# Optimization experiments

Hardware: AMD Instinct MI355X
Metric: run time of the kernel (lower is better)

Reference implementation:

```python
import jax, jax.numpy as jnp
import numpy as np

B, T, N, C = 2, 12, 4096, 32
FILTERS = [32, 32, 32]


def setup_inputs() -> dict:
    key = jax.random.key(0)
    ks = jax.random.split(key, 12)
    inp = {
        'data': jax.random.normal(ks[0], (B, T, N, C), dtype=jnp.float32),
        'adj': jax.random.uniform(ks[1], (3 * N, 3 * N), dtype=jnp.float32) / (3.0 * N),
        'temporal_emb': jax.random.normal(ks[2], (1, T, 1, C), dtype=jnp.float32) * 0.0003,
        'spatial_emb': jax.random.normal(ks[3], (1, 1, N, C), dtype=jnp.float32) * 0.0003,
    }
    c_in = C
    for i, f in enumerate(FILTERS):
        scale = 1.0 / np.sqrt(c_in)
        inp[f'W{i}'] = jax.random.uniform(ks[4 + 2 * i], (c_in, 2 * f), dtype=jnp.float32,
                                          minval=-scale, maxval=scale)
        inp[f'b{i}'] = jnp.zeros((2 * f,), dtype=jnp.float32)
        c_in = f
    return inp


def reference(data, adj, temporal_emb, spatial_emb, W0, b0, W1, b1, W2, b2):
    # data: (B, T, N, C). Add temporal + spatial position embeddings.
    x = data + temporal_emb + spatial_emb
    b, t, n, c = x.shape
    w = t - 2  # number of sliding windows
    # Gather all 3-step windows at once: (B, W, 3, N, C) -> (B, W, 3N, C)
    idx = jnp.arange(w)[:, None] + jnp.arange(3)[None, :]
    xw = x[:, idx].reshape(b, w, 3 * n, c)
    outs = []
    for Wl, bl in ((W0, b0), (W1, b1), (W2, b2)):
        # dense graph conv over the 3N local graph, batched over (B, W)
        xw = jnp.einsum('nm,bwmc->bwnc', adj, xw)
        y = xw @ Wl + bl            # (B, W, 3N, 2*C')
        lhs, rhs = jnp.split(y, 2, axis=-1)
        xw = lhs * jax.nn.sigmoid(rhs)  # GLU, (B, W, 3N, C')
        outs.append(xw[:, :, n:2 * n, :])  # crop middle timestep
    # stacked max over the gcn layers: (B, T-2, N, C_last)
    return jnp.max(jnp.stack(outs, axis=0), axis=0)
```

## Files before the change

kernel.cpp:

```cpp
#include <hip/hip_runtime.h>

#define NN 4096
#define TT 12
#define BB 2
#define CC 32
#define WW 10
#define K3 12288
#define NCOL 640
#define SA 4096.0f
#define SX 1024.0f

typedef _Float16 half8 __attribute__((ext_vector_type(8)));
typedef _Float16 half4_t __attribute__((ext_vector_type(4)));
typedef float floatx4 __attribute__((ext_vector_type(4)));

__global__ void k_conv_adj(const float* __restrict__ adj, _Float16* __restrict__ a16) {
    long n4 = (long)K3 * K3 / 4;
    long i = (long)blockIdx.x * blockDim.x + threadIdx.x;
    long stride = (long)gridDim.x * blockDim.x;
    const float4* src = (const float4*)adj;
    half4_t* dst = (half4_t*)a16;
    for (; i < n4; i += stride) {
        float4 v = src[i];
        half4_t h;
        h[0] = (_Float16)(v.x * SA);
        h[1] = (_Float16)(v.y * SA);
        h[2] = (_Float16)(v.z * SA);
        h[3] = (_Float16)(v.w * SA);
        dst[i] = h;
    }
}

__global__ void k_prep(const float* __restrict__ data, const float* __restrict__ temb,
                       const float* __restrict__ semb, _Float16* __restrict__ x0t) {
    __shared__ float sb[CC][64 + 1];
    int z = blockIdx.y;
    int b = z / 30; int r = z % 30; int w = r / 3; int j = r % 3;
    int t = w + j;
    int n0 = blockIdx.x * 64;
    int tid = threadIdx.x;
    for (int e = tid; e < 64 * CC; e += 256) {
        int nl = e >> 5, c = e & 31;
        float v = data[((long)(b * TT + t) * NN + n0 + nl) * CC + c]
                + temb[t * CC + c] + semb[(n0 + nl) * CC + c];
        sb[c][nl] = v;
    }
    __syncthreads();
    int bw = b * WW + w;
    for (int e = tid; e < 64 * CC; e += 256) {
        int c = e >> 6, nl = e & 63;
        x0t[(long)(bw * CC + c) * K3 + j * NN + n0 + nl] = (_Float16)sb[c][nl];
    }
}

__device__ __forceinline__ void gload_lds16(const _Float16* g, _Float16* l) {
    __builtin_amdgcn_global_load_lds(
        (const __attribute__((address_space(1))) void*)g,
        (__attribute__((address_space(3))) void*)l, 16, 0, 0);
}

__global__ __launch_bounds__(256, 2) void k_gemm(
    const _Float16* __restrict__ A, const _Float16* __restrict__ BT,
    float* __restrict__ G, int K)
{
    __shared__ __attribute__((aligned(16))) _Float16 As[128 * 32];
    __shared__ __attribute__((aligned(16))) _Float16 Bs[128 * 32];

    const int nbn = NCOL / 128;
    int nwg = gridDim.x;
    int cpx = nwg >> 3;
    int bid = blockIdx.x;
    int wg = (bid & 7) * cpx + (bid >> 3);
    int mt = wg / nbn, nt = wg - mt * nbn;
    long m0 = (long)mt * 128; long n0 = nt * 128;

    int tid = threadIdx.x;
    int lane = tid & 63, wid = tid >> 6;
    int wm = wid >> 1, wn = wid & 1;

    int rowS0 = tid >> 2, kb0 = tid & 3;
    int ks0 = kb0 ^ ((rowS0 >> 1) & 3);
    int s1 = tid + 256;
    int rowS1 = s1 >> 2, kb1 = s1 & 3;
    int ks1 = kb1 ^ ((rowS1 >> 1) & 3);

    const _Float16* aSrc0 = A + (m0 + rowS0) * (long)K + ks0 * 8;
    const _Float16* aSrc1 = A + (m0 + rowS1) * (long)K + ks1 * 8;
    const _Float16* bSrc0 = BT + (n0 + rowS0) * (long)K + ks0 * 8;
    const _Float16* bSrc1 = BT + (n0 + rowS1) * (long)K + ks1 * 8;

    floatx4 acc[4][4] = {};

    int arow = wm * 64 + (lane & 15);
    int brow = wn * 64 + (lane & 15);
    int ksr = lane >> 4;
    int kbA = ksr ^ ((arow >> 1) & 3);
    int kbB = ksr ^ ((brow >> 1) & 3);

#pragma unroll 1
    for (int k0 = 0; k0 < K; k0 += 32) {
        __syncthreads();
        gload_lds16(aSrc0 + k0, As + wid * 512);
        gload_lds16(aSrc1 + k0, As + 2048 + wid * 512);
        gload_lds16(bSrc0 + k0, Bs + wid * 512);
        gload_lds16(bSrc1 + k0, Bs + 2048 + wid * 512);
        asm volatile("s_waitcnt vmcnt(0)" ::: "memory");
        __syncthreads();

        half8 af[4], bf[4];
#pragma unroll
        for (int ms = 0; ms < 4; ++ms)
            af[ms] = *(const half8*)(As + (arow + ms * 16) * 32 + kbA * 8);
#pragma unroll
        for (int ns = 0; ns < 4; ++ns)
            bf[ns] = *(const half8*)(Bs + (brow + ns * 16) * 32 + kbB * 8);
#pragma unroll
        for (int ms = 0; ms < 4; ++ms)
#pragma unroll
            for (int ns = 0; ns < 4; ++ns)
                acc[ms][ns] = __builtin_amdgcn_mfma_f32_16x16x32_f16(af[ms], bf[ns], acc[ms][ns], 0, 0, 0);
    }

    int rb = (lane >> 4) * 4;
    int cb = lane & 15;
#pragma unroll
    for (int ms = 0; ms < 4; ++ms) {
        long row = m0 + wm * 64 + ms * 16 + rb;
#pragma unroll
        for (int ns = 0; ns < 4; ++ns) {
            long col = n0 + wn * 64 + ns * 16 + cb;
#pragma unroll
            for (int i = 0; i < 4; ++i)
                G[(row + i) * NCOL + col] = acc[ms][ns][i];
        }
    }
}

template <int MODE>
__global__ __launch_bounds__(256) void k_glu(
    const float* __restrict__ G, const float* __restrict__ Wt,
    const float* __restrict__ bias, _Float16* __restrict__ outH,
    float* __restrict__ outF, float invS, float outScale)
{
    __shared__ float Wl[CC * 64];
    __shared__ float bl[64];
    __shared__ _Float16 tb[4][CC][64];
    int tid = threadIdx.x;
    for (int e = tid; e < CC * 64; e += 256) Wl[e] = Wt[e];
    if (tid < 64) bl[tid] = bias[tid];
    __syncthreads();

    int blk = blockIdx.x;
    int mt = blk / 5, bwt = blk % 5;
    int m0 = mt * 64, bw0 = bwt * 4;
    int ml = tid >> 2, bwl = tid & 3;
    int m = m0 + ml, bw = bw0 + bwl;

    const float* gp = G + (long)m * NCOL + bw * CC;
    float g[CC];
#pragma unroll
    for (int c4 = 0; c4 < CC / 4; ++c4) {
        float4 v = ((const float4*)gp)[c4];
        g[c4 * 4 + 0] = v.x * invS; g[c4 * 4 + 1] = v.y * invS;
        g[c4 * 4 + 2] = v.z * invS; g[c4 * 4 + 3] = v.w * invS;
    }
    float y[64];
#pragma unroll
    for (int o = 0; o < 64; ++o) y[o] = bl[o];
#pragma unroll
    for (int c = 0; c < CC; ++c) {
        float gv = g[c];
#pragma unroll
        for (int o = 0; o < 64; ++o) y[o] = fmaf(gv, Wl[c * 64 + o], y[o]);
    }
    if (MODE == 0) {
#pragma unroll
        for (int c = 0; c < CC; ++c) {
            float r = y[c] * (1.f / (1.f + __expf(-y[c + 32])));
            tb[bwl][c][ml] = (_Float16)(r * outScale);
        }
        __syncthreads();
        for (int e = tid; e < 4 * CC * 64; e += 256) {
            int bwl2 = e >> 11, c2 = (e >> 6) & 31, ml2 = e & 63;
            outH[(long)((bw0 + bwl2) * CC + c2) * K3 + m0 + ml2] = tb[bwl2][c2][ml2];
        }
    } else {
        float* op = outF + (long)m * NCOL + bw * CC;
#pragma unroll
        for (int c = 0; c < CC; ++c) {
            float r = y[c] * (1.f / (1.f + __expf(-y[c + 32])));
            op[c] = r;
        }
    }
}

__global__ void k_final(const _Float16* __restrict__ x1t, const _Float16* __restrict__ x2t,
                        const float* __restrict__ o3, float* __restrict__ out)
{
    __shared__ float sb[64][CC + 1];
    int bw = blockIdx.y;
    int n0 = blockIdx.x * 64;
    int tid = threadIdx.x;
    for (int e = tid; e < CC * 64; e += 256) {
        int c = e >> 6, nl = e & 63;
        long idx = (long)(bw * CC + c) * K3 + NN + n0 + nl;
        float v1 = (float)x1t[idx] * (1.f / SX);
        float v2 = (float)x2t[idx] * (1.f / SX);
        sb[nl][c] = fmaxf(v1, v2);
    }
    __syncthreads();
    for (int e = tid; e < 64 * CC; e += 256) {
        int nl = e >> 5, c = e & 31;
        float v = fmaxf(sb[nl][c], o3[(long)(n0 + nl) * NCOL + bw * CC + c]);
        out[((long)bw * NN + n0 + nl) * CC + c] = v;
    }
}

extern "C" void kernel_launch(void* const* d_in, const int* in_sizes, int n_in,
                              void* d_out, int out_size, void* d_ws, size_t ws_size,
                              hipStream_t stream)
{
    const float* data = (const float*)d_in[0];
    const float* adj  = (const float*)d_in[1];
    const float* temb = (const float*)d_in[2];
    const float* semb = (const float*)d_in[3];
    const float* W0 = (const float*)d_in[4];
    const float* b0 = (const float*)d_in[5];
    const float* W1 = (const float*)d_in[6];
    const float* b1 = (const float*)d_in[7];
    const float* W2 = (const float*)d_in[8];
    const float* b2 = (const float*)d_in[9];
    float* out = (float*)d_out;

    char* ws = (char*)d_ws;
    _Float16* A16 = (_Float16*)ws;  ws += (size_t)K3 * K3 * 2;
    _Float16* X0  = (_Float16*)ws;  ws += (size_t)NCOL * K3 * 2;
    _Float16* X1  = (_Float16*)ws;  ws += (size_t)NCOL * K3 * 2;
    _Float16* X2  = (_Float16*)ws;  ws += (size_t)NCOL * K3 * 2;
    float*    G   = (float*)ws;     ws += (size_t)K3 * NCOL * 4;
    float*    O3  = (float*)ws;     ws += (size_t)NN * NCOL * 4;

    k_conv_adj<<<4096, 256, 0, stream>>>(adj, A16);
    k_prep<<<dim3(64, 60), 256, 0, stream>>>(data, temb, semb, X0);

    k_gemm<<<480, 256, 0, stream>>>(A16, X0, G, K3);
    k_glu<0><<<960, 256, 0, stream>>>(G, W0, b0, X1, nullptr, 1.f / SA, SX);
    k_gemm<<<480, 256, 0, stream>>>(A16, X1, G, K3);
    k_glu<0><<<960, 256, 0, stream>>>(G, W1, b1, X2, nullptr, 1.f / (SA * SX), SX);
    k_gemm<<<160, 256, 0, stream>>>(A16 + (size_t)NN * K3, X2, G, K3);
    k_glu<1><<<320, 256, 0, stream>>>(G, W2, b2, nullptr, O3, 1.f / (SA * SX), 1.f);

    k_final<<<dim3(64, 20), 256, 0, stream>>>(X1, X2, O3, out);
}
```

Measured before the change: 1.090 ms.

## Fuse GEMM with GLU epilogue and final max using full-width N tiles

Replaces the separate GEMM, GLU and final-max kernels with one fused kernel per layer. Each block computes a 48-row by all-640-column tile with double-buffered LDS staging, then runs the GLU weight multiply from LDS scratch and writes fp16 output directly. The last layer also folds in the max over the three layers. This removes the fp32 G round trips and extra launches, and reads A only once per layer instead of once per 128-column tile. In exchange, the grid is only 256 blocks (86 for the last layer) of 512 threads with large LDS use, which may cut occupancy. The LDS swizzle was also dropped, which may cause bank conflicts.

```diff
diff --git a/kernel.cpp b/kernel.cpp
--- a/kernel.cpp
+++ b/kernel.cpp
@@ -9,6 +9,9 @@
 #define NCOL 640
 #define SA 4096.0f
 #define SX 1024.0f
+#define BM 48
+#define BK 32
+#define NT (K3 / BK)
 
 typedef _Float16 half8 __attribute__((ext_vector_type(8)));
 typedef _Float16 half4_t __attribute__((ext_vector_type(4)));
@@ -59,161 +62,135 @@
         (__attribute__((address_space(3))) void*)l, 16, 0, 0);
 }
 
-__global__ __launch_bounds__(256, 2) void k_gemm(
+template <int MODE>
+__global__ __launch_bounds__(512, 2) void k_gemm_glu(
     const _Float16* __restrict__ A, const _Float16* __restrict__ BT,
-    float* __restrict__ G, int K)
+    const float* __restrict__ Wt, const float* __restrict__ bias,
+    _Float16* __restrict__ outH,
+    const _Float16* __restrict__ x1, const _Float16* __restrict__ x2,
+    float* __restrict__ outF,
+    float invS, int Mvalid)
 {
-    __shared__ __attribute__((aligned(16))) _Float16 As[128 * 32];
-    __shared__ __attribute__((aligned(16))) _Float16 Bs[128 * 32];
-
-    const int nbn = NCOL / 128;
-    int nwg = gridDim.x;
-    int cpx = nwg >> 3;
-    int bid = blockIdx.x;
-    int wg = (bid & 7) * cpx + (bid >> 3);
-    int mt = wg / nbn, nt = wg - mt * nbn;
-    long m0 = (long)mt * 128; long n0 = nt * 128;
+    __shared__ __attribute__((aligned(16))) _Float16 AB[2][22016];
+    __shared__ float WB[CC * 64 + 64];
 
     int tid = threadIdx.x;
     int lane = tid & 63, wid = tid >> 6;
-    int wm = wid >> 1, wn = wid & 1;
-
-    int rowS0 = tid >> 2, kb0 = tid & 3;
-    int ks0 = kb0 ^ ((rowS0 >> 1) & 3);
-    int s1 = tid + 256;
-    int rowS1 = s1 >> 2, kb1 = s1 & 3;
-    int ks1 = kb1 ^ ((rowS1 >> 1) & 3);
-
-    const _Float16* aSrc0 = A + (m0 + rowS0) * (long)K + ks0 * 8;
-    const _Float16* aSrc1 = A + (m0 + rowS1) * (long)K + ks1 * 8;
-    const _Float16* bSrc0 = BT + (n0 + rowS0) * (long)K + ks0 * 8;
-    const _Float16* bSrc1 = BT + (n0 + rowS1) * (long)K + ks1 * 8;
-
-    floatx4 acc[4][4] = {};
-
-    int arow = wm * 64 + (lane & 15);
-    int brow = wn * 64 + (lane & 15);
-    int ksr = lane >> 4;
-    int kbA = ksr ^ ((arow >> 1) & 3);
-    int kbB = ksr ^ ((brow >> 1) & 3);
-
+    long m0 = (long)blockIdx.x * BM;
+
+    for (int e = tid; e < CC * 64; e += 512) WB[e] = Wt[e];
+    if (tid < 64) WB[CC * 64 + tid] = bias[tid];
+
+    int rowA = tid >> 2, kbA = tid & 3;
+    const _Float16* aSrc = A + (m0 + rowA) * (long)K3 + kbA * 8;
+    const _Float16* bSrc0 = BT + (long)((0 * 512 + tid) >> 2) * K3 + ((0 * 512 + tid) & 3) * 8;
+    const _Float16* bSrc1 = BT + (long)((1 * 512 + tid) >> 2) * K3 + ((1 * 512 + tid) & 3) * 8;
+    const _Float16* bSrc2 = BT + (long)((2 * 512 + tid) >> 2) * K3 + ((2 * 512 + tid) & 3) * 8;
+    const _Float16* bSrc3 = BT + (long)((3 * 512 + tid) >> 2) * K3 + ((3 * 512 + tid) & 3) * 8;
+    const _Float16* bSrc4 = BT + (long)((4 * 512 + tid) >> 2) * K3 + ((4 * 512 + tid) & 3) * 8;
+
+#define STAGE(bufi, tt)                                                          \
+    do {                                                                         \
+        long k0 = (long)(tt) * BK;                                               \
+        _Float16* bp = AB[bufi];                                                 \
+        gload_lds16(bSrc0 + k0, bp + 1536 + 0 * 4096 + wid * 512);               \
+        gload_lds16(bSrc1 + k0, bp + 1536 + 1 * 4096 + wid * 512);               \
+        gload_lds16(bSrc2 + k0, bp + 1536 + 2 * 4096 + wid * 512);               \
+        gload_lds16(bSrc3 + k0, bp + 1536 + 3 * 4096 + wid * 512);               \
+        gload_lds16(bSrc4 + k0, bp + 1536 + 4 * 4096 + wid * 512);               \
+        if (wid < 3) gload_lds16(aSrc + k0, bp + wid * 512);                     \
+    } while (0)
+
+    floatx4 acc[3][5] = {};
+    int fr = lane & 15;
+    int kq = lane >> 4;
+
+    STAGE(0, 0);
+    asm volatile("s_waitcnt vmcnt(0)" ::: "memory");
+    __syncthreads();
+
+    int cur = 0;
 #pragma unroll 1
-    for (int k0 = 0; k0 < K; k0 += 32) {
-        __syncthreads();
-        gload_lds16(aSrc0 + k0, As + wid * 512);
-        gload_lds16(aSrc1 + k0, As + 2048 + wid * 512);
-        gload_lds16(bSrc0 + k0, Bs + wid * 512);
-        gload_lds16(bSrc1 + k0, Bs + 2048 + wid * 512);
+    for (int t = 0; t < NT; ++t) {
+        if (t != NT - 1) STAGE(cur ^ 1, t + 1);
+        const _Float16* P = AB[cur];
+        half8 af[3], bf[5];
+#pragma unroll
+        for (int ms = 0; ms < 3; ++ms)
+            af[ms] = *(const half8*)(P + (ms * 16 + fr) * 32 + kq * 8);
+#pragma unroll
+        for (int ns = 0; ns < 5; ++ns)
+            bf[ns] = *(const half8*)(P + 1536 + (wid * 80 + ns * 16 + fr) * 32 + kq * 8);
+#pragma unroll
+        for (int ms = 0; ms < 3; ++ms)
+#pragma unroll
+            for (int ns = 0; ns < 5; ++ns)
+                acc[ms][ns] = __builtin_amdgcn_mfma_f32_16x16x32_f16(af[ms], bf[ns], acc[ms][ns], 0, 0, 0);
         asm volatile("s_waitcnt vmcnt(0)" ::: "memory");
         __syncthreads();
-
-        half8 af[4], bf[4];
-#pragma unroll
-        for (int ms = 0; ms < 4; ++ms)
-            af[ms] = *(const half8*)(As + (arow + ms * 16) * 32 + kbA * 8);
-#pragma unroll
-        for (int ns = 0; ns < 4; ++ns)
-            bf[ns] = *(const half8*)(Bs + (brow + ns * 16) * 32 + kbB * 8);
-#pragma unroll
-        for (int ms = 0; ms < 4; ++ms)
-#pragma unroll
-            for (int ns = 0; ns < 4; ++ns)
-                acc[ms][ns] = __builtin_amdgcn_mfma_f32_16x16x32_f16(af[ms], bf[ns], acc[ms][ns], 0, 0, 0);
-    }
-
-    int rb = (lane >> 4) * 4;
-    int cb = lane & 15;
-#pragma unroll
-    for (int ms = 0; ms < 4; ++ms) {
-        long row = m0 + wm * 64 + ms * 16 + rb;
-#pragma unroll
-        for (int ns = 0; ns < 4; ++ns) {
-            long col = n0 + wn * 64 + ns * 16 + cb;
-#pragma unroll
-            for (int i = 0; i < 4; ++i)
-                G[(row + i) * NCOL + col] = acc[ms][ns][i];
-        }
-    }
-}
-
-template <int MODE>
-__global__ __launch_bounds__(256) void k_glu(
-    const float* __restrict__ G, const float* __restrict__ Wt,
-    const float* __restrict__ bias, _Float16* __restrict__ outH,
-    float* __restrict__ outF, float invS, float outScale)
-{
-    __shared__ float Wl[CC * 64];
-    __shared__ float bl[64];
-    __shared__ _Float16 tb[4][CC][64];
-    int tid = threadIdx.x;
-    for (int e = tid; e < CC * 64; e += 256) Wl[e] = Wt[e];
-    if (tid < 64) bl[tid] = bias[tid];
-    __syncthreads();
-
-    int blk = blockIdx.x;
-    int mt = blk / 5, bwt = blk % 5;
-    int m0 = mt * 64, bw0 = bwt * 4;
-    int ml = tid >> 2, bwl = tid & 3;
-    int m = m0 + ml, bw = bw0 + bwl;
-
-    const float* gp = G + (long)m * NCOL + bw * CC;
-    float g[CC];
-#pragma unroll
-    for (int c4 = 0; c4 < CC / 4; ++c4) {
-        float4 v = ((const float4*)gp)[c4];
-        g[c4 * 4 + 0] = v.x * invS; g[c4 * 4 + 1] = v.y * invS;
-        g[c4 * 4 + 2] = v.z * invS; g[c4 * 4 + 3] = v.w * invS;
-    }
-    float y[64];
-#pragma unroll
-    for (int o = 0; o < 64; ++o) y[o] = bl[o];
-#pragma unroll
-    for (int c = 0; c < CC; ++c) {
-        float gv = g[c];
-#pragma unroll
-        for (int o = 0; o < 64; ++o) y[o] = fmaf(gv, Wl[c * 64 + o], y[o]);
-    }
-    if (MODE == 0) {
-#pragma unroll
-        for (int c = 0; c < CC; ++c) {
-            float r = y[c] * (1.f / (1.f + __expf(-y[c + 32])));
-            tb[bwl][c][ml] = (_Float16)(r * outScale);
+        cur ^= 1;
+    }
+
+    float* scr = (float*)AB;
+    const int SCRW = 321;
+    int rb = (lane >> 4) * 4, cb = lane & 15;
+
+#pragma unroll 1
+    for (int h = 0; h < 2; ++h) {
+        __syncthreads();
+        if ((wid >> 2) == h) {
+            int wl = wid & 3;
+#pragma unroll
+            for (int ms = 0; ms < 3; ++ms)
+#pragma unroll
+                for (int ns = 0; ns < 5; ++ns)
+#pragma unroll
+                    for (int i = 0; i < 4; ++i)
+                        scr[(ms * 16 + rb + i) * SCRW + wl * 80 + ns * 16 + cb] = acc[ms][ns][i];
         }
         __syncthreads();
-        for (int e = tid; e < 4 * CC * 64; e += 256) {
-            int bwl2 = e >> 11, c2 = (e >> 6) & 31, ml2 = e & 63;
-            outH[(long)((bw0 + bwl2) * CC + c2) * K3 + m0 + ml2] = tb[bwl2][c2][ml2];
+        if (tid < 480) {
+            int row = tid % 48;
+            int bwl = tid / 48;
+            int bw = h * 10 + bwl;
+            long m = m0 + row;
+            float g[CC];
+#pragma unroll
+            for (int c = 0; c < CC; ++c) g[c] = scr[row * SCRW + bwl * 32 + c] * invS;
+            float y[64];
+#pragma unroll
+            for (int o = 0; o < 64; ++o) y[o] = WB[CC * 64 + o];
+#pragma unroll
+            for (int c = 0; c < CC; ++c) {
+                float gv = g[c];
+#pragma unroll
+                for (int o = 0; o < 64; ++o) y[o] = fmaf(gv, WB[c * 64 + o], y[o]);
+            }
+            if (MODE == 0) {
+#pragma unroll
+                for (int c = 0; c < CC; ++c) {
+                    float r = y[c] * (1.f / (1.f + __expf(-y[c + 32])));
+                    outH[(long)(bw * CC + c) * K3 + m] = (_Float16)(r * SX);
+                }
+            } else {
+                if (m < Mvalid) {
+                    float res[CC];
+#pragma unroll
+                    for (int c = 0; c < CC; ++c) {
+                        float r = y[c] * (1.f / (1.f + __expf(-y[c + 32])));
+                        float v1 = (float)x1[(long)(bw * CC + c) * K3 + NN + m] * (1.f / SX);
+                        float v2 = (float)x2[(long)(bw * CC + c) * K3 + NN + m] * (1.f / SX);
+                        res[c] = fmaxf(r, fmaxf(v1, v2));
+                    }
+                    float4* op = (float4*)(outF + ((long)bw * NN + m) * CC);
+#pragma unroll
+                    for (int q = 0; q < CC / 4; ++q)
+                        op[q] = make_float4(res[q * 4 + 0], res[q * 4 + 1], res[q * 4 + 2], res[q * 4 + 3]);
+                }
+            }
         }
-    } else {
-        float* op = outF + (long)m * NCOL + bw * CC;
-#pragma unroll
-        for (int c = 0; c < CC; ++c) {
-            float r = y[c] * (1.f / (1.f + __expf(-y[c + 32])));
-            op[c] = r;
-        }
-    }
-}
-
-__global__ void k_final(const _Float16* __restrict__ x1t, const _Float16* __restrict__ x2t,
-                        const float* __restrict__ o3, float* __restrict__ out)
-{
-    __shared__ float sb[64][CC + 1];
-    int bw = blockIdx.y;
-    int n0 = blockIdx.x * 64;
-    int tid = threadIdx.x;
-    for (int e = tid; e < CC * 64; e += 256) {
-        int c = e >> 6, nl = e & 63;
-        long idx = (long)(bw * CC + c) * K3 + NN + n0 + nl;
-        float v1 = (float)x1t[idx] * (1.f / SX);
-        float v2 = (float)x2t[idx] * (1.f / SX);
-        sb[nl][c] = fmaxf(v1, v2);
-    }
-    __syncthreads();
-    for (int e = tid; e < 64 * CC; e += 256) {
-        int nl = e >> 5, c = e & 31;
-        float v = fmaxf(sb[nl][c], o3[(long)(n0 + nl) * NCOL + bw * CC + c]);
-        out[((long)bw * NN + n0 + nl) * CC + c] = v;
-    }
+    }
+#undef STAGE
 }
 
 extern "C" void kernel_launch(void* const* d_in, const int* in_sizes, int n_in,
@@ -231,24 +208,21 @@
     const float* W2 = (const float*)d_in[8];
     const float* b2 = (const float*)d_in[9];
     float* out = (float*)d_out;
+    (void)ws_size; (void)in_sizes; (void)n_in; (void)out_size;
 
     char* ws = (char*)d_ws;
     _Float16* A16 = (_Float16*)ws;  ws += (size_t)K3 * K3 * 2;
     _Float16* X0  = (_Float16*)ws;  ws += (size_t)NCOL * K3 * 2;
     _Float16* X1  = (_Float16*)ws;  ws += (size_t)NCOL * K3 * 2;
     _Float16* X2  = (_Float16*)ws;  ws += (size_t)NCOL * K3 * 2;
-    float*    G   = (float*)ws;     ws += (size_t)K3 * NCOL * 4;
-    float*    O3  = (float*)ws;     ws += (size_t)NN * NCOL * 4;
 
     k_conv_adj<<<4096, 256, 0, stream>>>(adj, A16);
     k_prep<<<dim3(64, 60), 256, 0, stream>>>(data, temb, semb, X0);
 
-    k_gemm<<<480, 256, 0, stream>>>(A16, X0, G, K3);
-    k_glu<0><<<960, 256, 0, stream>>>(G, W0, b0, X1, nullptr, 1.f / SA, SX);
-    k_gemm<<<480, 256, 0, stream>>>(A16, X1, G, K3);
-    k_glu<0><<<960, 256, 0, stream>>>(G, W1, b1, X2, nullptr, 1.f / (SA * SX), SX);
-    k_gemm<<<160, 256, 0, stream>>>(A16 + (size_t)NN * K3, X2, G, K3);
-    k_glu<1><<<320, 256, 0, stream>>>(G, W2, b2, nullptr, O3, 1.f / (SA * SX), 1.f);
-
-    k_final<<<dim3(64, 20), 256, 0, stream>>>(X1, X2, O3, out);
-}
+    k_gemm_glu<0><<<256, 512, 0, stream>>>(A16, X0, W0, b0, X1,
+                                           nullptr, nullptr, nullptr, 1.f / SA, K3);
+    k_gemm_glu<0><<<256, 512, 0, stream>>>(A16, X1, W1, b1, X2,
+                                           nullptr, nullptr, nullptr, 1.f / (SA * SX), K3);
+    k_gemm_glu<1><<<86, 512, 0, stream>>>(A16 + (size_t)NN * K3, X2, W2, b2, nullptr,
+                                          X1, X2, out, 1.f / (SA * SX), NN);
+}
```

New measurement: 1.613 ms. 1.48x slower.
